# Performance work log

Hardware: AMD Instinct MI355X
Metric: run time of the kernel (lower is better)

## Reference

```python
import jax, jax.numpy as jnp
import numpy as np

EMBED = 256; HEADS = 8; LEVELS = 1; POINTS = 4; QUEUE = 2
HB = 200; WB = 200; NQ = HB * WB; BS = 1


def bilinear_sample(img, grid, h, w):
    # img: (BH, D, h*w) flattened feature map; grid: (BH, N, 2) in [-1, 1]
    # torch.grid_sample(align_corners=False, padding_mode='zeros') semantics
    gx, gy = grid[..., 0], grid[..., 1]
    x = (gx + 1.0) * (w * 0.5) - 0.5
    y = (gy + 1.0) * (h * 0.5) - 0.5
    x0 = jnp.floor(x); y0 = jnp.floor(y)
    lx = x - x0; ly = y - y0
    x0i = x0.astype(jnp.int32); y0i = y0.astype(jnp.int32)

    def corner(xi, yi, wgt):
        valid = ((xi >= 0) & (xi < w) & (yi >= 0) & (yi < h)).astype(img.dtype)
        idx = jnp.clip(yi, 0, h - 1) * w + jnp.clip(xi, 0, w - 1)  # (BH, N)
        vals = jax.vmap(lambda im, ix: im[:, ix])(img, idx)  # (BH, D, N)
        return vals * (wgt * valid)[:, None, :]

    return (corner(x0i, y0i, (1 - lx) * (1 - ly))
            + corner(x0i + 1, y0i, lx * (1 - ly))
            + corner(x0i, y0i + 1, (1 - lx) * ly)
            + corner(x0i + 1, y0i + 1, lx * ly))


def ms_deform_attn(value, shapes, loc, aw):
    # value: (B, Nv, H, D); loc: (B, nq, H, L, P, 2); aw: (B, nq, H, L, P)
    B, Nv, H, D = value.shape
    nq = loc.shape[1]; P = loc.shape[4]
    grids = 2.0 * loc - 1.0
    start = 0
    per_level = []
    for l in range(shapes.shape[0]):
        h, w = int(shapes[l, 0]), int(shapes[l, 1])
        vl = value[:, start:start + h * w].reshape(B, h, w, H, D)
        vl = vl.transpose(0, 3, 4, 1, 2).reshape(B * H, D, h * w)
        g = grids[:, :, :, l].transpose(0, 2, 1, 3, 4).reshape(B * H, nq * P, 2)
        samp = bilinear_sample(vl, g, h, w).reshape(B, H, D, nq, P)
        per_level.append(samp)
        start += h * w
    sampled = jnp.stack(per_level, axis=4)  # (B, H, D, nq, L, P)
    w_ = aw.transpose(0, 2, 1, 3, 4)[:, :, None]  # (B, H, 1, nq, L, P)
    out = (sampled * w_).sum(axis=(-1, -2))  # (B, H, D, nq)
    return out.reshape(B, H * D, nq).transpose(0, 2, 1)  # (B, nq, E)


def setup_inputs():
    key = jax.random.key(0)
    ks = jax.random.split(key, 10)
    s = 0.02
    n_off = QUEUE * HEADS * LEVELS * POINTS * 2
    n_aw = QUEUE * HEADS * LEVELS * POINTS
    return {
        "query": jax.random.normal(ks[0], (BS, NQ, EMBED), jnp.float32),
        "query_pos": jax.random.normal(ks[1], (BS, NQ, EMBED), jnp.float32),
        "value": jax.random.normal(ks[2], (BS * QUEUE, NQ, EMBED), jnp.float32),
        "reference_points": jax.random.uniform(ks[3], (BS * QUEUE, NQ, LEVELS, 2), jnp.float32),
        "spatial_shapes": jnp.array([[HB, WB]], dtype=jnp.int32),
        "W_off": jax.random.normal(ks[4], (EMBED * QUEUE, n_off), jnp.float32) * s,
        "b_off": jnp.zeros((n_off,), jnp.float32),
        "W_attn": jax.random.normal(ks[5], (EMBED * QUEUE, n_aw), jnp.float32) * s,
        "b_attn": jnp.zeros((n_aw,), jnp.float32),
        "W_val": jax.random.normal(ks[6], (EMBED, EMBED), jnp.float32) * s,
        "b_val": jnp.zeros((EMBED,), jnp.float32),
        "W_out": jax.random.normal(ks[7], (EMBED, EMBED), jnp.float32) * s,
        "b_out": jnp.zeros((EMBED,), jnp.float32),
    }


def reference(query, query_pos, value, reference_points, spatial_shapes,
              W_off, b_off, W_attn, b_attn, W_val, b_val, W_out, b_out):
    shapes = np.asarray(spatial_shapes)  # static level shapes
    bs, nq, E = query.shape
    identity = query
    q = query + query_pos
    # temporal query: concat current-frame value with query
    q2 = jnp.concatenate([value[:bs], q], axis=-1)  # (bs, nq, 2E)
    v = value @ W_val + b_val  # (bs*2, nv, E)
    nv = v.shape[1]
    v = v.reshape(bs * QUEUE, nv, HEADS, E // HEADS)
    off = (q2 @ W_off + b_off).reshape(bs, nq, HEADS, QUEUE, LEVELS, POINTS, 2)
    aw = (q2 @ W_attn + b_attn).reshape(bs, nq, HEADS, QUEUE, LEVELS * POINTS)
    aw = jax.nn.softmax(aw, axis=-1).reshape(bs, nq, HEADS, QUEUE, LEVELS, POINTS)
    aw = aw.transpose(0, 3, 1, 2, 4, 5).reshape(bs * QUEUE, nq, HEADS, LEVELS, POINTS)
    off = off.transpose(0, 3, 1, 2, 4, 5, 6).reshape(bs * QUEUE, nq, HEADS, LEVELS, POINTS, 2)
    # normalized sampling locations: (bs*2, nq, H, L, P, 2)
    normalizer = jnp.stack([spatial_shapes[..., 1], spatial_shapes[..., 0]], -1).astype(jnp.float32)
    loc = reference_points[:, :, None, :, None, :] + off / normalizer[None, None, None, :, None, :]
    out = ms_deform_attn(v, shapes, loc, aw)  # (bs*2, nq, E)
    # average over the BEV queue (current + history)
    out = out.transpose(1, 2, 0).reshape(nq, E, bs, QUEUE).mean(-1).transpose(2, 0, 1)
    out = out @ W_out + b_out
    return out + identity
```

## Files before the change

kernel.cpp:

```cpp
#include <hip/hip_runtime.h>
#include <math.h>

#define NQ    40000
#define EMB   256
#define NHEAD 8
#define HDIM  32
#define HB    200
#define WB    200
#define NCOL  192

typedef __attribute__((ext_vector_type(8))) __bf16 bf16x8;
typedef __attribute__((ext_vector_type(4))) float f32x4;

static __device__ __forceinline__ unsigned short f2bf(float f) {
  unsigned u = __float_as_uint(f);
  u = u + 0x7fffu + ((u >> 16) & 1u);
  return (unsigned short)(u >> 16);
}
static __device__ __forceinline__ float bf2f(unsigned short s) {
  return __uint_as_float(((unsigned)s) << 16);
}

__global__ __launch_bounds__(256) void conv_w(
    const float* __restrict__ W_off, const float* __restrict__ b_off,
    const float* __restrict__ W_attn, const float* __restrict__ b_attn,
    const float* __restrict__ W_val, const float* __restrict__ W_out,
    unsigned short* __restrict__ Wc1t, unsigned short* __restrict__ Wvt,
    unsigned short* __restrict__ Wot, float* __restrict__ bc1)
{
  int idx = blockIdx.x * 256 + threadIdx.x;
  if (idx < 98304) {
    int n = idx >> 9, k = idx & 511;
    float v = (n < 128) ? W_off[(size_t)k * 128 + n] : W_attn[(size_t)k * 64 + (n - 128)];
    Wc1t[idx] = f2bf(v);
  } else if (idx < 163840) {
    int j = idx - 98304;
    int n = j >> 8, k = j & 255;
    Wvt[j] = f2bf(W_val[(size_t)k * 256 + n]);
  } else if (idx < 229376) {
    int j = idx - 163840;
    int n = j >> 8, k = j & 255;
    Wot[j] = f2bf(W_out[(size_t)k * 256 + n]);
  } else if (idx < 229568) {
    int n = idx - 229376;
    bc1[n] = (n < 128) ? b_off[n] : b_attn[n - 128];
  }
}

template<int K, int N, int AMODE, int OMODE, bool RESID>
__global__ __launch_bounds__(256) void rb_gemm(
    const void* __restrict__ Aptr, const void* __restrict__ Aq2a,
    const void* __restrict__ Aq2b, const unsigned short* __restrict__ Bt,
    const float* __restrict__ bias, const float* __restrict__ resid,
    void* __restrict__ outp)
{
  constexpr int NFR = N / 64;
  constexpr int NP  = N + 8;
  constexpr int ATB = (AMODE != 0) ? 32 * K * 2 : 0;
  constexpr int TRB = (OMODE == 1) ? 32 * NP * 2 : 0;
  constexpr int MXB = (ATB > TRB) ? ATB : TRB;
  constexpr int LDSB = (MXB > 64) ? MXB : 64;
  __shared__ __align__(16) char lds[LDSB];
  unsigned short* trn = (unsigned short*)lds;

  const int t = threadIdx.x;
  const int m0 = blockIdx.x * 32;
  const int wid = t >> 6, lane = t & 63;
  const int wn = wid * (N / 4);
  const int lr = lane & 15, quad = lane >> 4;

  if constexpr (AMODE != 0) {
    constexpr int CH  = K / 8;
    constexpr int NST = (32 * CH) / 256;
    #pragma unroll
    for (int l = 0; l < NST; l++) {
      int ci = t + l * 256;
      int r = ci / CH, c = ci % CH;
      int grow = m0 + r;
      float4 f0, f1;
      if constexpr (AMODE == 1) {
        const float* s = (const float*)Aptr + (size_t)grow * K + c * 8;
        f0 = *(const float4*)s; f1 = *(const float4*)(s + 4);
      } else {
        if (c < 32) {
          const float* s = (const float*)Aptr + (size_t)grow * 256 + c * 8;
          f0 = *(const float4*)s; f1 = *(const float4*)(s + 4);
        } else {
          const float* sq = (const float*)Aq2a + (size_t)grow * 256 + (c - 32) * 8;
          const float* sp = (const float*)Aq2b + (size_t)grow * 256 + (c - 32) * 8;
          float4 a0 = *(const float4*)sq, a1 = *(const float4*)(sq + 4);
          float4 b0 = *(const float4*)sp, b1 = *(const float4*)(sp + 4);
          f0 = make_float4(a0.x + b0.x, a0.y + b0.y, a0.z + b0.z, a0.w + b0.w);
          f1 = make_float4(a1.x + b1.x, a1.y + b1.y, a1.z + b1.z, a1.w + b1.w);
        }
      }
      union { unsigned short us[8]; uint4 v; } u;
      u.us[0] = f2bf(f0.x); u.us[1] = f2bf(f0.y);
      u.us[2] = f2bf(f0.z); u.us[3] = f2bf(f0.w);
      u.us[4] = f2bf(f1.x); u.us[5] = f2bf(f1.y);
      u.us[6] = f2bf(f1.z); u.us[7] = f2bf(f1.w);
      *(uint4*)(lds + (size_t)r * (K * 2) + ((c ^ (r & 7)) * 16)) = u.v;
    }
    __syncthreads();
  }

  f32x4 acc[2][NFR];
  #pragma unroll
  for (int i = 0; i < 2; i++)
    #pragma unroll
    for (int n = 0; n < NFR; n++) acc[i][n] = (f32x4){0.f, 0.f, 0.f, 0.f};

  #pragma unroll 2
  for (int k0 = 0; k0 < K; k0 += 32) {
    const int kf = k0 + quad * 8;
    bf16x8 bfr[NFR];
    #pragma unroll
    for (int n = 0; n < NFR; n++)
      bfr[n] = *(const bf16x8*)(Bt + (size_t)(wn + n * 16 + lr) * K + kf);

    bf16x8 af[2];
    if constexpr (AMODE == 0) {
      const unsigned short* A = (const unsigned short*)Aptr;
      #pragma unroll
      for (int i = 0; i < 2; i++)
        af[i] = *(const bf16x8*)(A + (size_t)(m0 + lr + i * 16) * K + kf);
    } else {
      const int cb = kf >> 3;
      const int sw = (cb ^ (lr & 7)) * 16;
      #pragma unroll
      for (int i = 0; i < 2; i++)
        af[i] = *(const bf16x8*)(lds + (size_t)(lr + i * 16) * (K * 2) + sw);
    }
    #pragma unroll
    for (int i = 0; i < 2; i++)
      #pragma unroll
      for (int n = 0; n < NFR; n++)
        acc[i][n] = __builtin_amdgcn_mfma_f32_16x16x32_bf16(af[i], bfr[n], acc[i][n], 0, 0, 0);
  }

  if constexpr (OMODE == 0) {
    #pragma unroll
    for (int i = 0; i < 2; i++) {
      int rowb = m0 + i * 16 + quad * 4;
      #pragma unroll
      for (int n = 0; n < NFR; n++) {
        int col = wn + n * 16 + lr;
        float bsv = bias[col];
        #pragma unroll
        for (int r = 0; r < 4; r++) {
          int rr = rowb + r;
          float v = acc[i][n][r] + bsv;
          if (RESID) v += resid[(size_t)rr * N + col];
          ((float*)outp)[(size_t)rr * N + col] = v;
        }
      }
    }
  } else {
    if constexpr (AMODE != 0) __syncthreads();
    #pragma unroll
    for (int i = 0; i < 2; i++) {
      #pragma unroll
      for (int n = 0; n < NFR; n++) {
        int col = wn + n * 16 + lr;
        float bsv = bias[col];
        #pragma unroll
        for (int r = 0; r < 4; r++) {
          int rl = i * 16 + quad * 4 + r;
          trn[rl * NP + col] = f2bf(acc[i][n][r] + bsv);
        }
      }
    }
    __syncthreads();
    constexpr int NCH = (32 * N) / 2048;
    #pragma unroll
    for (int l = 0; l < NCH; l++) {
      int c = t + l * 256;
      int row = c / (N / 8);
      int coloff = (c % (N / 8)) * 8;
      uint4 d = *(const uint4*)(trn + row * NP + coloff);
      *(uint4*)((unsigned short*)outp + (size_t)(m0 + row) * N + coloff) = d;
    }
  }
}

__global__ __launch_bounds__(256) void k3_sample(
    const unsigned short* __restrict__ raw1, const float* __restrict__ refp,
    const unsigned short* __restrict__ v, unsigned short* __restrict__ msd)
{
  __shared__ int4   sidx[2][64];
  __shared__ float4 swgt[2][64];
  const int t = threadIdx.x;
  const int q0 = blockIdx.x * 2;

  if (t < 128) {
    const int s = t >> 6, e = t & 63;
    const int b = e >> 5, h = (e >> 2) & 7, p = e & 3;
    const int q = q0 + s;
    const unsigned short* r = raw1 + (size_t)q * NCOL;
    float ox = bf2f(r[h * 16 + b * 8 + p * 2 + 0]);
    float oy = bf2f(r[h * 16 + b * 8 + p * 2 + 1]);
    float l0 = bf2f(r[128 + h * 8 + b * 4 + 0]);
    float l1 = bf2f(r[128 + h * 8 + b * 4 + 1]);
    float l2 = bf2f(r[128 + h * 8 + b * 4 + 2]);
    float l3 = bf2f(r[128 + h * 8 + b * 4 + 3]);
    float mx = fmaxf(fmaxf(l0, l1), fmaxf(l2, l3));
    float e0 = expf(l0 - mx), e1 = expf(l1 - mx);
    float e2 = expf(l2 - mx), e3 = expf(l3 - mx);
    float ssum = e0 + e1 + e2 + e3;
    float ep = (p == 0) ? e0 : (p == 1) ? e1 : (p == 2) ? e2 : e3;
    float aw = ep / ssum * 0.5f;
    float rx = refp[((size_t)b * NQ + q) * 2 + 0];
    float ry = refp[((size_t)b * NQ + q) * 2 + 1];
    float px = rx * (float)WB + ox - 0.5f;
    float py = ry * (float)HB + oy - 0.5f;
    float x0f = floorf(px), y0f = floorf(py);
    float lx = px - x0f, ly = py - y0f;
    int x0 = (int)x0f, y0 = (int)y0f, x1 = x0 + 1, y1 = y0 + 1;
    int x0c = min(max(x0, 0), WB - 1), x1c = min(max(x1, 0), WB - 1);
    int y0c = min(max(y0, 0), HB - 1), y1c = min(max(y1, 0), HB - 1);
    float vx0 = ((unsigned)x0 < (unsigned)WB) ? 1.f : 0.f;
    float vx1 = ((unsigned)x1 < (unsigned)WB) ? 1.f : 0.f;
    float vy0 = ((unsigned)y0 < (unsigned)HB) ? 1.f : 0.f;
    float vy1 = ((unsigned)y1 < (unsigned)HB) ? 1.f : 0.f;
    const int pb = b * NQ;
    const int hb = h * HDIM;
    int4 ix;
    ix.x = (pb + y0c * WB + x0c) * EMB + hb;
    ix.y = (pb + y0c * WB + x1c) * EMB + hb;
    ix.z = (pb + y1c * WB + x0c) * EMB + hb;
    ix.w = (pb + y1c * WB + x1c) * EMB + hb;
    float4 wv;
    wv.x = aw * (1.f - lx) * (1.f - ly) * vx0 * vy0;
    wv.y = aw * lx * (1.f - ly) * vx1 * vy0;
    wv.z = aw * (1.f - lx) * ly * vx0 * vy1;
    wv.w = aw * lx * ly * vx1 * vy1;
    sidx[s][e] = ix;
    swgt[s][e] = wv;
  }
  __syncthreads();

  const int s = t >> 7, u = t & 127;
  const int h = u >> 4, d2 = u & 15;
  const unsigned short* vd = v + d2 * 2;
  float a0 = 0.f, a1 = 0.f;
  #pragma unroll
  for (int b = 0; b < 2; b++) {
    #pragma unroll
    for (int p = 0; p < 4; p++) {
      int ent = b * 32 + h * 4 + p;
      int4 ix = sidx[s][ent];
      float4 wv = swgt[s][ent];
      unsigned c00 = *(const unsigned*)(vd + ix.x);
      unsigned c10 = *(const unsigned*)(vd + ix.y);
      unsigned c01 = *(const unsigned*)(vd + ix.z);
      unsigned c11 = *(const unsigned*)(vd + ix.w);
      a0 += wv.x * __uint_as_float(c00 << 16);
      a1 += wv.x * __uint_as_float(c00 & 0xffff0000u);
      a0 += wv.y * __uint_as_float(c10 << 16);
      a1 += wv.y * __uint_as_float(c10 & 0xffff0000u);
      a0 += wv.z * __uint_as_float(c01 << 16);
      a1 += wv.z * __uint_as_float(c01 & 0xffff0000u);
      a0 += wv.w * __uint_as_float(c11 << 16);
      a1 += wv.w * __uint_as_float(c11 & 0xffff0000u);
    }
  }
  unsigned pack = ((unsigned)f2bf(a1) << 16) | (unsigned)f2bf(a0);
  *(unsigned*)(msd + (size_t)(q0 + s) * EMB + h * HDIM + d2 * 2) = pack;
}

extern "C" void kernel_launch(void* const* d_in, const int* in_sizes, int n_in,
                              void* d_out, int out_size, void* d_ws, size_t ws_size,
                              hipStream_t stream) {
  const float* query     = (const float*)d_in[0];
  const float* query_pos = (const float*)d_in[1];
  const float* value     = (const float*)d_in[2];
  const float* refp      = (const float*)d_in[3];
  const float* W_off  = (const float*)d_in[5];
  const float* b_off  = (const float*)d_in[6];
  const float* W_attn = (const float*)d_in[7];
  const float* b_attn = (const float*)d_in[8];
  const float* W_val  = (const float*)d_in[9];
  const float* b_val  = (const float*)d_in[10];
  const float* W_out  = (const float*)d_in[11];
  const float* b_out  = (const float*)d_in[12];
  float* out = (float*)d_out;

  char* ws = (char*)d_ws;
  unsigned short* raw1 = (unsigned short*)(ws);
  unsigned short* vout = (unsigned short*)(ws + 15360000);
  unsigned short* msdb = (unsigned short*)(ws + 56320000);
  unsigned short* Wc1t = (unsigned short*)(ws + 76800000);
  unsigned short* Wvt  = (unsigned short*)(ws + 76996608);
  unsigned short* Wot  = (unsigned short*)(ws + 77127680);
  float*          bc1  = (float*)(ws + 77258752);

  hipLaunchKernelGGL(conv_w, dim3(897), dim3(256), 0, stream,
                     W_off, b_off, W_attn, b_attn, W_val, W_out, Wc1t, Wvt, Wot, bc1);

  hipLaunchKernelGGL((rb_gemm<512, 192, 2, 1, false>),
                     dim3(1250), dim3(256), 0, stream,
                     (const void*)value, (const void*)query, (const void*)query_pos,
                     Wc1t, bc1, (const float*)nullptr, (void*)raw1);
  hipLaunchKernelGGL((rb_gemm<256, 256, 1, 1, false>),
                     dim3(2500), dim3(256), 0, stream,
                     (const void*)value, (const void*)nullptr, (const void*)nullptr,
                     Wvt, b_val, (const float*)nullptr, (void*)vout);
  hipLaunchKernelGGL(k3_sample, dim3(NQ / 2), dim3(256), 0, stream,
                     raw1, refp, vout, msdb);
  hipLaunchKernelGGL((rb_gemm<256, 256, 0, 0, true>),
                     dim3(1250), dim3(256), 0, stream,
                     (const void*)msdb, (const void*)nullptr, (const void*)nullptr,
                     Wot, b_out, query, (void*)out);
}
```

Measured before the change: 374.8 us.

## Software-pipeline GEMM K loop and batch A-tile global loads before conversion

Restructures the A-tile staging so each thread issues all of its global float4 loads up front before converting them to bf16 and storing to LDS, which raises memory-level parallelism. The K loop is fully unrolled and double-buffers the B and A fragments, so the loads for step k+1 are in flight while the MFMAs for step k run. Launch bounds now request 4 blocks per SM to limit register use. The extra live fragments raise register pressure, and the occupancy hint could force spills.

Result: faster. 366.4 us (-2.3%).

```diff
diff --git a/kernel.cpp b/kernel.cpp
--- a/kernel.cpp
+++ b/kernel.cpp
@@ -48,7 +48,7 @@
 }
 
 template<int K, int N, int AMODE, int OMODE, bool RESID>
-__global__ __launch_bounds__(256) void rb_gemm(
+__global__ __launch_bounds__(256, 4) void rb_gemm(
     const void* __restrict__ Aptr, const void* __restrict__ Aq2a,
     const void* __restrict__ Aq2b, const unsigned short* __restrict__ Bt,
     const float* __restrict__ bias, const float* __restrict__ resid,
@@ -69,37 +69,61 @@
   const int wn = wid * (N / 4);
   const int lr = lane & 15, quad = lane >> 4;
 
-  if constexpr (AMODE != 0) {
-    constexpr int CH  = K / 8;
-    constexpr int NST = (32 * CH) / 256;
-    #pragma unroll
-    for (int l = 0; l < NST; l++) {
-      int ci = t + l * 256;
-      int r = ci / CH, c = ci % CH;
-      int grow = m0 + r;
-      float4 f0, f1;
-      if constexpr (AMODE == 1) {
-        const float* s = (const float*)Aptr + (size_t)grow * K + c * 8;
-        f0 = *(const float4*)s; f1 = *(const float4*)(s + 4);
-      } else {
-        if (c < 32) {
-          const float* s = (const float*)Aptr + (size_t)grow * 256 + c * 8;
-          f0 = *(const float4*)s; f1 = *(const float4*)(s + 4);
-        } else {
-          const float* sq = (const float*)Aq2a + (size_t)grow * 256 + (c - 32) * 8;
-          const float* sp = (const float*)Aq2b + (size_t)grow * 256 + (c - 32) * 8;
-          float4 a0 = *(const float4*)sq, a1 = *(const float4*)(sq + 4);
-          float4 b0 = *(const float4*)sp, b1 = *(const float4*)(sp + 4);
-          f0 = make_float4(a0.x + b0.x, a0.y + b0.y, a0.z + b0.z, a0.w + b0.w);
-          f1 = make_float4(a1.x + b1.x, a1.y + b1.y, a1.z + b1.z, a1.w + b1.w);
+  auto cvt_store = [&](int r, int c, float4 f0, float4 f1) {
+    union { unsigned short us[8]; uint4 v; } u;
+    u.us[0] = f2bf(f0.x); u.us[1] = f2bf(f0.y);
+    u.us[2] = f2bf(f0.z); u.us[3] = f2bf(f0.w);
+    u.us[4] = f2bf(f1.x); u.us[5] = f2bf(f1.y);
+    u.us[6] = f2bf(f1.z); u.us[7] = f2bf(f1.w);
+    *(uint4*)(lds + (size_t)r * (K * 2) + ((c ^ (r & 7)) * 16)) = u.v;
+  };
+
+  if constexpr (AMODE == 1) {
+    const int c = t & 31, r0 = t >> 5;
+    float4 f[4][2];
+    #pragma unroll
+    for (int l = 0; l < 4; l++) {
+      const float* s = (const float*)Aptr + (size_t)(m0 + r0 + 8 * l) * K + c * 8;
+      f[l][0] = *(const float4*)s; f[l][1] = *(const float4*)(s + 4);
+    }
+    #pragma unroll
+    for (int l = 0; l < 4; l++)
+      cvt_store(r0 + 8 * l, c, f[l][0], f[l][1]);
+    __syncthreads();
+  } else if constexpr (AMODE == 2) {
+    const int c = t & 63, r0 = t >> 6;
+    if (c < 32) {
+      float4 f[8][2];
+      #pragma unroll
+      for (int l = 0; l < 8; l++) {
+        const float* s = (const float*)Aptr + (size_t)(m0 + r0 + 4 * l) * 256 + c * 8;
+        f[l][0] = *(const float4*)s; f[l][1] = *(const float4*)(s + 4);
+      }
+      #pragma unroll
+      for (int l = 0; l < 8; l++)
+        cvt_store(r0 + 4 * l, c, f[l][0], f[l][1]);
+    } else {
+      #pragma unroll
+      for (int h = 0; h < 2; h++) {
+        float4 fq[4][2], fp[4][2];
+        #pragma unroll
+        for (int l = 0; l < 4; l++) {
+          int r = r0 + 4 * (h * 4 + l);
+          const float* sq = (const float*)Aq2a + (size_t)(m0 + r) * 256 + (c - 32) * 8;
+          const float* sp = (const float*)Aq2b + (size_t)(m0 + r) * 256 + (c - 32) * 8;
+          fq[l][0] = *(const float4*)sq; fq[l][1] = *(const float4*)(sq + 4);
+          fp[l][0] = *(const float4*)sp; fp[l][1] = *(const float4*)(sp + 4);
+        }
+        #pragma unroll
+        for (int l = 0; l < 4; l++) {
+          int r = r0 + 4 * (h * 4 + l);
+          float4 f0 = make_float4(fq[l][0].x + fp[l][0].x, fq[l][0].y + fp[l][0].y,
+                                  fq[l][0].z + fp[l][0].z, fq[l][0].w + fp[l][0].w);
+          float4 f1 = make_float4(fq[l][1].x + fp[l][1].x, fq[l][1].y + fp[l][1].y,
+                                  fq[l][1].z + fp[l][1].z, fq[l][1].w + fp[l][1].w);
+          cvt_store(r, c, f0, f1);
         }
       }
-      union { unsigned short us[8]; uint4 v; } u;
-      u.us[0] = f2bf(f0.x); u.us[1] = f2bf(f0.y);
-      u.us[2] = f2bf(f0.z); u.us[3] = f2bf(f0.w);
-      u.us[4] = f2bf(f1.x); u.us[5] = f2bf(f1.y);
-      u.us[6] = f2bf(f1.z); u.us[7] = f2bf(f1.w);
-      *(uint4*)(lds + (size_t)r * (K * 2) + ((c ^ (r & 7)) * 16)) = u.v;
     }
     __syncthreads();
   }
@@ -110,32 +134,47 @@
     #pragma unroll
     for (int n = 0; n < NFR; n++) acc[i][n] = (f32x4){0.f, 0.f, 0.f, 0.f};
 
-  #pragma unroll 2
-  for (int k0 = 0; k0 < K; k0 += 32) {
-    const int kf = k0 + quad * 8;
-    bf16x8 bfr[NFR];
+  auto loadB = [&](bf16x8* dst, int k0) {
     #pragma unroll
     for (int n = 0; n < NFR; n++)
-      bfr[n] = *(const bf16x8*)(Bt + (size_t)(wn + n * 16 + lr) * K + kf);
-
-    bf16x8 af[2];
+      dst[n] = *(const bf16x8*)(Bt + (size_t)(wn + n * 16 + lr) * K + k0 + quad * 8);
+  };
+  auto loadA = [&](bf16x8* dst, int k0) {
     if constexpr (AMODE == 0) {
       const unsigned short* A = (const unsigned short*)Aptr;
       #pragma unroll
       for (int i = 0; i < 2; i++)
-        af[i] = *(const bf16x8*)(A + (size_t)(m0 + lr + i * 16) * K + kf);
+        dst[i] = *(const bf16x8*)(A + (size_t)(m0 + lr + i * 16) * K + k0 + quad * 8);
     } else {
-      const int cb = kf >> 3;
+      const int cb = (k0 >> 3) + quad;
       const int sw = (cb ^ (lr & 7)) * 16;
       #pragma unroll
       for (int i = 0; i < 2; i++)
-        af[i] = *(const bf16x8*)(lds + (size_t)(lr + i * 16) * (K * 2) + sw);
+        dst[i] = *(const bf16x8*)(lds + (size_t)(lr + i * 16) * (K * 2) + sw);
+    }
+  };
+
+  constexpr int NK = K / 32;
+  bf16x8 bcur[NFR], af[2];
+  loadB(bcur, 0);
+  loadA(af, 0);
+  #pragma unroll
+  for (int ks = 0; ks < NK; ks++) {
+    bf16x8 bnxt[NFR], anxt[2];
+    if (ks + 1 < NK) {
+      loadB(bnxt, (ks + 1) * 32);
+      loadA(anxt, (ks + 1) * 32);
     }
     #pragma unroll
     for (int i = 0; i < 2; i++)
       #pragma unroll
       for (int n = 0; n < NFR; n++)
-        acc[i][n] = __builtin_amdgcn_mfma_f32_16x16x32_bf16(af[i], bfr[n], acc[i][n], 0, 0, 0);
+        acc[i][n] = __builtin_amdgcn_mfma_f32_16x16x32_bf16(af[i], bcur[n], acc[i][n], 0, 0, 0);
+    if (ks + 1 < NK) {
+      #pragma unroll
+      for (int n = 0; n < NFR; n++) bcur[n] = bnxt[n];
+      af[0] = anxt[0]; af[1] = anxt[1];
+    }
   }
 
   if constexpr (OMODE == 0) {
```
